# Performance work log

Hardware: AMD Instinct MI355X
Metric: run time of the kernel (lower is better)

## Reference

```python
import jax, jax.numpy as jnp
import numpy as np

N = 100_000
IN_CH = 256
OUT_CH = 128
KVOL = 8  # 2^3 kernel offsets for kernel_size=2, dimension=3


def setup_inputs() -> dict:
    key = jax.random.key(0)
    k1, k2, k3 = jax.random.split(key, 3)
    feats = jax.random.normal(k1, (N, IN_CH), dtype=jnp.float32)
    coords = jax.random.randint(k2, (N, 3), 0, 512, dtype=jnp.int32)
    # ME transpose-conv kernel layout: [kernel_volume, in_ch, out_ch]
    W = jax.random.normal(k3, (KVOL, IN_CH, OUT_CH), dtype=jnp.float32) * (1.0 / np.sqrt(IN_CH * KVOL))
    return {"feats": feats, "coords": coords, "W": W}


def reference(feats, coords, W):
    # Sparse transposed conv, kernel_size=2, stride=2, dim=3.
    # Because kernel == stride, kernel offsets tile the output lattice disjointly:
    # each input voxel at coord c emits 8 output voxels at 2*c + offset, offset in {0,1}^3,
    # with features x_i @ W_k.  This is the gather-GEMM-scatter with a trivially
    # bijective kernel map, so no accumulation collisions occur.
    # out_feats[n, k, :] = feats[n, :] @ W[k, :, :]
    out = jnp.einsum('nc,kcd->nkd', feats, W)          # [N, 8, OUT_CH]
    out_feats = out.reshape(-1, OUT_CH)                 # [8N, OUT_CH]
    # Output coordinates (stride halved): 2*c + offset (returned for completeness).
    offs = jnp.stack(jnp.meshgrid(*([jnp.arange(2, dtype=coords.dtype)] * 3),
                                  indexing='ij'), axis=-1).reshape(KVOL, 3)  # [8,3]
    out_coords = (coords[:, None, :] * 2 + offs[None, :, :]).reshape(-1, 3)  # [8N,3]
    return out_feats, out_coords
```

## Files before the change

### kernel.cpp

```cpp
#include <hip/hip_runtime.h>


#define N_PTS  100000
#define CIN    256
#define COUT   128
#define KVOL   8
#define NCOL   1024
#define MT     128
#define LDA    264
#define FEATS_OUT_ELEMS 102400000
#define COORD_OUT_ELEMS 2400000

typedef __bf16 bf16x8 __attribute__((ext_vector_type(8)));
typedef float  f32x4  __attribute__((ext_vector_type(4)));
typedef unsigned short u16;
typedef u16 u16x8 __attribute__((ext_vector_type(8)));
typedef u16 u16x4 __attribute__((ext_vector_type(4)));

__device__ __forceinline__ u16 f2bf(float x) {
  unsigned u = __builtin_bit_cast(unsigned, x);
  u += 0x7FFFu + ((u >> 16) & 1u);
  return (u16)(u >> 16);
}

__global__ void prep_w_kernel(const float* __restrict__ W, u16* __restrict__ Wt) {
  __shared__ float t[32][33];
  int bx = blockIdx.x;
  int k  = bx >> 5;
  int ct = (bx & 31) >> 2;
  int dt = bx & 3;
  int c0 = ct * 32, d0 = dt * 32;
  int tx = threadIdx.x & 31, ty = threadIdx.x >> 5;
  const float* Wk = W + (size_t)k * (CIN * COUT);
#pragma unroll
  for (int i = 0; i < 4; ++i) {
    int c = ty + i * 8;
    t[c][tx] = Wk[(size_t)(c0 + c) * COUT + d0 + tx];
  }
  __syncthreads();
  u16* Wtk = Wt + (size_t)k * (CIN * COUT);
#pragma unroll
  for (int i = 0; i < 4; ++i) {
    int d = ty + i * 8;
    Wtk[(size_t)(d0 + d) * CIN + c0 + tx] = f2bf(t[tx][d]);
  }
}

__global__ void coords_kernel(const int* __restrict__ coords, float* __restrict__ outc) {
  int idx = blockIdx.x * 256 + threadIdx.x;
  if (idx >= COORD_OUT_ELEMS) return;
  int n = idx / 24;
  int r = idx - n * 24;
  int k = r / 3;
  int t = r - k * 3;
  int bit = (k >> (2 - t)) & 1;
  outc[idx] = (float)(2 * coords[n * 3 + t] + bit);
}

__global__ __launch_bounds__(256, 1) void gemm_kernel(const float* __restrict__ feats,
                                                      const u16* __restrict__ Wt,
                                                      float* __restrict__ out) {
  __shared__ u16 As[MT * LDA];
  __shared__ u16 Bs[COUT * LDA];
  const int tid = threadIdx.x;
  const int m0  = blockIdx.x * MT;

#pragma unroll
  for (int i = 0; i < 32; ++i) {
    int f   = tid + i * 256;
    int row = f >> 6;
    int c4  = (f & 63) << 2;
    int gr  = m0 + row;
    float4 v = make_float4(0.f, 0.f, 0.f, 0.f);
    if (gr < N_PTS) v = *(const float4*)(feats + (size_t)gr * CIN + c4);
    u16x4 p;
    p.x = f2bf(v.x); p.y = f2bf(v.y); p.z = f2bf(v.z); p.w = f2bf(v.w);
    *(u16x4*)&As[row * LDA + c4] = p;
  }

  const int lane = tid & 63;
  const int wave = tid >> 6;
  const int wrow = (wave & 1) << 6;
  const int wcol = (wave >> 1) << 6;
  const int lr   = lane & 15;
  const int quad = lane >> 4;

  for (int kv = 0; kv < KVOL; ++kv) {
    __syncthreads();
    const u16* Wk = Wt + kv * (CIN * COUT);
#pragma unroll
    for (int i = 0; i < 16; ++i) {
      int ch  = tid + i * 256;
      int row = ch >> 5;
      int c8  = (ch & 31) << 3;
      u16x8 v = *(const u16x8*)(Wk + (size_t)row * CIN + c8);
      *(u16x8*)&Bs[row * LDA + c8] = v;
    }
    __syncthreads();

    f32x4 acc[4][4];
#pragma unroll
    for (int r = 0; r < 4; ++r)
#pragma unroll
      for (int c = 0; c < 4; ++c)
        acc[r][c] = f32x4{0.f, 0.f, 0.f, 0.f};

#pragma unroll
    for (int ks = 0; ks < 8; ++ks) {
      const int ko = ks * 32 + quad * 8;
      bf16x8 a[4], b[4];
#pragma unroll
      for (int r = 0; r < 4; ++r)
        a[r] = __builtin_bit_cast(bf16x8, *(const u16x8*)&As[(wrow + r * 16 + lr) * LDA + ko]);
#pragma unroll
      for (int c = 0; c < 4; ++c)
        b[c] = __builtin_bit_cast(bf16x8, *(const u16x8*)&Bs[(wcol + c * 16 + lr) * LDA + ko]);
#pragma unroll
      for (int r = 0; r < 4; ++r)
#pragma unroll
        for (int c = 0; c < 4; ++c)
          acc[r][c] = __builtin_amdgcn_mfma_f32_16x16x32_bf16(a[r], b[c], acc[r][c], 0, 0, 0);
    }

    const int colbase = (kv << 7) + wcol + lr;
#pragma unroll
    for (int r = 0; r < 4; ++r) {
      const int rowb = m0 + wrow + r * 16 + quad * 4;
#pragma unroll
      for (int c = 0; c < 4; ++c) {
        const int col = colbase + c * 16;
#pragma unroll
        for (int q = 0; q < 4; ++q) {
          const int row = rowb + q;
          if (row < N_PTS) out[(size_t)row * NCOL + col] = acc[r][c][q];
        }
      }
    }
  }
}

extern "C" void kernel_launch(void* const* d_in, const int* in_sizes, int n_in,
                              void* d_out, int out_size, void* d_ws, size_t ws_size,
                              hipStream_t stream) {
  const float* feats  = (const float*)d_in[0];
  const int*   coords = (const int*)d_in[1];
  const float* W      = (const float*)d_in[2];
  float* out = (float*)d_out;
  u16*   Wt  = (u16*)d_ws;

  prep_w_kernel<<<256, 256, 0, stream>>>(W, Wt);
  coords_kernel<<<(COORD_OUT_ELEMS + 255) / 256, 256, 0, stream>>>(coords, out + (size_t)FEATS_OUT_ELEMS);
  gemm_kernel<<<(N_PTS + MT - 1) / MT, 256, 0, stream>>>(feats, Wt, out);
}
```

Measured before the change: 623.7 us.

## Read weights directly from global, swap MFMA operands for vector nontemporal stores

Drops the shared-memory staging of each weight slice and its two barriers per kernel offset, so B fragments now load straight from global (L2-cached) memory. The MFMA operand order is swapped so each lane holds four consecutive output columns, which allows 16-byte nontemporal vector stores in place of scalar stores. Launch bounds are raised to two blocks per CU, enabled by the smaller LDS footprint. The trade-off is that weight loads now go to global memory on every k-step, which adds memory latency inside the MFMA loop.

```diff
diff --git a/kernel.cpp b/kernel.cpp
--- a/kernel.cpp
+++ b/kernel.cpp
@@ -57,11 +57,10 @@
   outc[idx] = (float)(2 * coords[n * 3 + t] + bit);
 }
 
-__global__ __launch_bounds__(256, 1) void gemm_kernel(const float* __restrict__ feats,
+__global__ __launch_bounds__(256, 2) void gemm_kernel(const float* __restrict__ feats,
                                                       const u16* __restrict__ Wt,
                                                       float* __restrict__ out) {
   __shared__ u16 As[MT * LDA];
-  __shared__ u16 Bs[COUT * LDA];
   const int tid = threadIdx.x;
   const int m0  = blockIdx.x * MT;
 
@@ -77,6 +76,7 @@
     p.x = f2bf(v.x); p.y = f2bf(v.y); p.z = f2bf(v.z); p.w = f2bf(v.w);
     *(u16x4*)&As[row * LDA + c4] = p;
   }
+  __syncthreads();
 
   const int lane = tid & 63;
   const int wave = tid >> 6;
@@ -86,17 +86,7 @@
   const int quad = lane >> 4;
 
   for (int kv = 0; kv < KVOL; ++kv) {
-    __syncthreads();
     const u16* Wk = Wt + kv * (CIN * COUT);
-#pragma unroll
-    for (int i = 0; i < 16; ++i) {
-      int ch  = tid + i * 256;
-      int row = ch >> 5;
-      int c8  = (ch & 31) << 3;
-      u16x8 v = *(const u16x8*)(Wk + (size_t)row * CIN + c8);
-      *(u16x8*)&Bs[row * LDA + c8] = v;
-    }
-    __syncthreads();
 
     f32x4 acc[4][4];
 #pragma unroll
@@ -114,26 +104,24 @@
         a[r] = __builtin_bit_cast(bf16x8, *(const u16x8*)&As[(wrow + r * 16 + lr) * LDA + ko]);
 #pragma unroll
       for (int c = 0; c < 4; ++c)
-        b[c] = __builtin_bit_cast(bf16x8, *(const u16x8*)&Bs[(wcol + c * 16 + lr) * LDA + ko]);
+        b[c] = __builtin_bit_cast(bf16x8,
+                 *(const u16x8*)(Wk + (size_t)(wcol + c * 16 + lr) * CIN + ko));
 #pragma unroll
       for (int r = 0; r < 4; ++r)
 #pragma unroll
         for (int c = 0; c < 4; ++c)
-          acc[r][c] = __builtin_amdgcn_mfma_f32_16x16x32_bf16(a[r], b[c], acc[r][c], 0, 0, 0);
+          acc[r][c] = __builtin_amdgcn_mfma_f32_16x16x32_bf16(b[c], a[r], acc[r][c], 0, 0, 0);
     }
 
-    const int colbase = (kv << 7) + wcol + lr;
+    const int cb = (kv << 7) + wcol + (quad << 2);
 #pragma unroll
     for (int r = 0; r < 4; ++r) {
-      const int rowb = m0 + wrow + r * 16 + quad * 4;
+      const int row = m0 + wrow + r * 16 + lr;
+      if (row < N_PTS) {
+        float* orow = out + (size_t)row * NCOL + cb;
 #pragma unroll
-      for (int c = 0; c < 4; ++c) {
-        const int col = colbase + c * 16;
-#pragma unroll
-        for (int q = 0; q < 4; ++q) {
-          const int row = rowb + q;
-          if (row < N_PTS) out[(size_t)row * NCOL + col] = acc[r][c][q];
-        }
+        for (int c = 0; c < 4; ++c)
+          __builtin_nontemporal_store(acc[r][c], (f32x4*)(orow + c * 16));
       }
     }
   }
```

Result: no change. 621.3 us (-0.4%).
